# Kernel tuning notes

Hardware: AMD Instinct MI355X
Metric: run time of the kernel (lower is better)

Reference implementation:

```python
import jax, jax.numpy as jnp
import numpy as np

HID = 128
N_NODES = 50000
N_EDGES = 640000
N_GRAPHS = 64
N_LAYERS = 3
LN_EPS = 1e-5


def _ln(h, g, b):
    mu = jnp.mean(h, axis=-1, keepdims=True)
    v = jnp.mean(jnp.square(h - mu), axis=-1, keepdims=True)
    return (h - mu) * jax.lax.rsqrt(v + LN_EPS) * g + b


def _mlp2(h, W1, b1, g, be, W2, b2):
    # Linear -> ReLU -> LayerNorm -> (Dropout=identity in eval) -> Linear
    h = _ln(jax.nn.relu(h @ W1.T + b1), g, be)
    return h @ W2.T + b2


def _forward(x, edge_index, batch, axis_W1, axis_b1, axis_g, axis_be, axis_W2, axis_b2, org_W1, org_b1, org_g, org_be, org_W2, org_b2, nin_W, nin_b, conv_W1, conv_b1, conv_g, conv_be, conv_W2, conv_b2, eps, ln_g, ln_b, gate_W1, gate_b1, gate_g, gate_be, gate_W2, gate_b2, head_W1, head_b1, head_g, head_be, head_W2, head_b2):
    axis = x[:, 9:12]
    origin = x[:, 12:15]
    others = jnp.concatenate([x[:, :9], x[:, 15:19]], axis=1)  # [N, 13]
    axis_z = _mlp2(axis, axis_W1, axis_b1, axis_g, axis_be, axis_W2, axis_b2)
    org_z = _mlp2(origin, org_W1, org_b1, org_g, org_be, org_W2, org_b2)
    h = jnp.concatenate([others, axis_z, org_z], axis=1) @ nin_W.T + nin_b  # [N, HID]
    src, dst = edge_index[0], edge_index[1]
    n = x.shape[0]
    for l in range(N_LAYERS):
        res = h
        # GIN: sum-aggregate source features into targets (gather + scatter-add)
        agg = jax.ops.segment_sum(h[src], dst, num_segments=n)
        m = (1.0 + eps[l]) * h + agg
        m = _mlp2(m, conv_W1[l], conv_b1[l], conv_g[l], conv_be[l], conv_W2[l], conv_b2[l])
        h = _ln(jax.nn.relu(m), ln_g[l], ln_b[l]) + res
    # AttentionalAggregation: segment softmax over per-graph node gates
    gate = _mlp2(h, gate_W1, gate_b1, gate_g, gate_be, gate_W2, gate_b2)  # [N, 1]
    gmax = jax.ops.segment_max(gate, batch, num_segments=N_GRAPHS)
    e = jnp.exp(gate - gmax[batch])
    denom = jax.ops.segment_sum(e, batch, num_segments=N_GRAPHS)
    attn = e / denom[batch]
    g = jax.ops.segment_sum(attn * h, batch, num_segments=N_GRAPHS)  # [B, HID]
    logit = _mlp2(g, head_W1, head_b1, head_g, head_be, head_W2, head_b2)[:, 0]
    return logit


def setup_inputs() -> dict:
    key = jax.random.key(0)
    ks = iter(jax.random.split(key, 64))
    nk = lambda: next(ks)
    lin = lambda o, i: jax.random.normal(nk(), (o, i), jnp.float32) / np.float32(np.sqrt(i))
    lin3 = lambda L, o, i: jnp.stack([lin(o, i) for _ in range(L)])
    z = lambda *s: jnp.zeros(s, jnp.float32)
    o = lambda *s: jnp.ones(s, jnp.float32)
    inp = {}
    inp['x'] = jax.random.normal(nk(), (N_NODES, 19), jnp.float32)
    inp['edge_index'] = jax.random.randint(nk(), (2, N_EDGES), 0, N_NODES)
    inp['batch'] = jnp.sort(jax.random.randint(nk(), (N_NODES,), 0, N_GRAPHS))
    for p in ('axis', 'org'):
        inp[p + '_W1'] = lin(16, 3); inp[p + '_b1'] = z(16)
        inp[p + '_g'] = o(16); inp[p + '_be'] = z(16)
        inp[p + '_W2'] = lin(16, 16); inp[p + '_b2'] = z(16)
    inp['nin_W'] = lin(HID, 45); inp['nin_b'] = z(HID)
    inp['conv_W1'] = lin3(N_LAYERS, HID, HID); inp['conv_b1'] = z(N_LAYERS, HID)
    inp['conv_g'] = o(N_LAYERS, HID); inp['conv_be'] = z(N_LAYERS, HID)
    inp['conv_W2'] = lin3(N_LAYERS, HID, HID); inp['conv_b2'] = z(N_LAYERS, HID)
    inp['eps'] = z(N_LAYERS)
    inp['ln_g'] = o(N_LAYERS, HID); inp['ln_b'] = z(N_LAYERS, HID)
    for p in ('gate', 'head'):
        inp[p + '_W1'] = lin(HID // 2, HID); inp[p + '_b1'] = z(HID // 2)
        inp[p + '_g'] = o(HID // 2); inp[p + '_be'] = z(HID // 2)
        inp[p + '_W2'] = lin(1, HID // 2); inp[p + '_b2'] = z(1)
    return inp


def reference(x, edge_index, batch, axis_W1, axis_b1, axis_g, axis_be, axis_W2, axis_b2, org_W1, org_b1, org_g, org_be, org_W2, org_b2, nin_W, nin_b, conv_W1, conv_b1, conv_g, conv_be, conv_W2, conv_b2, eps, ln_g, ln_b, gate_W1, gate_b1, gate_g, gate_be, gate_W2, gate_b2, head_W1, head_b1, head_g, head_be, head_W2, head_b2):
    return _forward(x, edge_index, batch, axis_W1, axis_b1, axis_g, axis_be, axis_W2, axis_b2, org_W1, org_b1, org_g, org_be, org_W2, org_b2, nin_W, nin_b, conv_W1, conv_b1, conv_g, conv_be, conv_W2, conv_b2, eps, ln_g, ln_b, gate_W1, gate_b1, gate_g, gate_be, gate_W2, gate_b2, head_W1, head_b1, head_g, head_be, head_W2, head_b2)
```

## Files before the change

kernel.cpp:

```cpp
#include <hip/hip_runtime.h>

#define N_NODESC 50000
#define N_EDGESC 640000
#define N_GRAPHSC 64
#define HIDC 128
#define LN_EPSF 1e-5f
#define POOL_SPLIT 16
#define SCAN_NB 49
#define EGRID ((N_EDGESC + 255) / 256)
#define NGRID_GB ((N_NODESC + 255) / 256)
#define WPREP_NB 32

typedef short bf16x8 __attribute__((ext_vector_type(8)));
typedef float f32x4 __attribute__((ext_vector_type(4)));

static __device__ __forceinline__ unsigned ord_enc(float f) {
  unsigned u = __float_as_uint(f);
  return (u & 0x80000000u) ? ~u : (u | 0x80000000u);
}
static __device__ __forceinline__ float ord_dec(unsigned u) {
  return __uint_as_float((u & 0x80000000u) ? (u ^ 0x80000000u) : ~u);
}
static __device__ __forceinline__ unsigned short f2bf(float x) {
  unsigned u = __float_as_uint(x);
  u += 0x7fffu + ((u >> 16) & 1u);
  return (unsigned short)(u >> 16);
}
static __device__ __forceinline__ float bf2f(unsigned short b) {
  return __uint_as_float(((unsigned)b) << 16);
}

static __device__ __forceinline__ void mlp16(float in0, float in1, float in2,
    const float* __restrict__ W1, const float* __restrict__ b1,
    const float* __restrict__ g, const float* __restrict__ be,
    const float* __restrict__ W2, const float* __restrict__ b2,
    float* __restrict__ out) {
  float h[16];
  float s1 = 0.f, s2 = 0.f;
#pragma unroll
  for (int j = 0; j < 16; ++j) {
    float v = b1[j] + W1[j*3+0]*in0 + W1[j*3+1]*in1 + W1[j*3+2]*in2;
    v = fmaxf(v, 0.f);
    h[j] = v; s1 += v; s2 += v*v;
  }
  float mu = s1 * (1.f/16.f);
  float var = fmaxf(s2 * (1.f/16.f) - mu*mu, 0.f);
  float rs = rsqrtf(var + LN_EPSF);
  float z[16];
#pragma unroll
  for (int j = 0; j < 16; ++j) z[j] = (h[j]-mu)*rs*g[j] + be[j];
#pragma unroll
  for (int j = 0; j < 16; ++j) {
    float v = b2[j];
#pragma unroll
    for (int k = 0; k < 16; ++k) v += W2[j*16+k]*z[k];
    out[j] = v;
  }
}

__global__ __launch_bounds__(256) void hist_gbound_kernel(const int* __restrict__ ei,
    int* __restrict__ deg, const int* __restrict__ batch, int* __restrict__ gstart,
    const float* __restrict__ ninW, unsigned short* __restrict__ ninWb) {
  const int b = blockIdx.x;
  if (b < EGRID) {
    int e = b * 256 + threadIdx.x;
    if (e < N_EDGESC) atomicAdd(&deg[ei[N_EDGESC + e]], 1);
  } else if (b < EGRID + NGRID_GB) {
    int i = (b - EGRID) * 256 + threadIdx.x;
    if (i >= N_NODESC) return;
    int bb = batch[i];
    int prev = (i == 0) ? -1 : batch[i-1];
    for (int g = prev + 1; g <= bb; ++g) gstart[g] = i;
    if (i == N_NODESC - 1) {
      for (int g = bb + 1; g <= N_GRAPHSC; ++g) gstart[g] = N_NODESC;
    }
  } else {
    int i = (b - EGRID - NGRID_GB) * 256 + threadIdx.x;
    if (i < 128*64) {
      int f = i >> 6, k = i & 63;
      ninWb[i] = (k < 45) ? f2bf(ninW[f*45 + k]) : (unsigned short)0;
    }
  }
}

__global__ __launch_bounds__(1024) void scan1_kernel(const int* __restrict__ deg,
                                                     int* __restrict__ incl,
                                                     int* __restrict__ bsum) {
  const int b = blockIdx.x, t = threadIdx.x;
  const int i = b * 1024 + t;
  const int lane = t & 63, w = t >> 6;
  int v = (i < N_NODESC) ? deg[i] : 0;
#pragma unroll
  for (int off = 1; off < 64; off <<= 1) {
    int n = __shfl_up(v, off);
    if (lane >= off) v += n;
  }
  __shared__ int wsum[16];
  if (lane == 63) wsum[w] = v;
  __syncthreads();
  if (t == 0) {
    int run = 0;
#pragma unroll
    for (int k = 0; k < 16; ++k) { int x = wsum[k]; wsum[k] = run; run += x; }
  }
  __syncthreads();
  v += wsum[w];
  if (i < N_NODESC) incl[i] = v;
  if (t == 1023) bsum[b] = v;
}

__global__ __launch_bounds__(1024) void scan23_kernel(const int* __restrict__ deg,
                                                      const int* __restrict__ bsum,
                                                      int* __restrict__ rowptr,
                                                      int* __restrict__ cursor) {
  __shared__ int ex[SCAN_NB + 1];
  const int b = blockIdx.x, t = threadIdx.x;
  if (t < 64) {
    int v = (t < SCAN_NB) ? bsum[t] : 0;
    const int orig = v;
#pragma unroll
    for (int off = 1; off < 64; off <<= 1) {
      int n = __shfl_up(v, off);
      if (t >= off) v += n;
    }
    if (t < SCAN_NB) ex[t] = v - orig;
    if (t == SCAN_NB - 1) ex[SCAN_NB] = v;
  }
  __syncthreads();
  const int i = b * 1024 + t;
  if (i < N_NODESC) {
    int excl = rowptr[i] - deg[i] + ex[b];
    rowptr[i] = excl;
    cursor[i] = excl;
  }
  if (b == 0 && t == 0) rowptr[N_NODESC] = ex[SCAN_NB];
}

__global__ __launch_bounds__(256) void scatter_kernel(const int* __restrict__ ei,
                                                      int* __restrict__ cursor,
                                                      int* __restrict__ esrc) {
  int e = blockIdx.x * 256 + threadIdx.x;
  if (e < N_EDGESC) {
    int d = ei[N_EDGESC + e];
    int slot = atomicAdd(&cursor[d], 1);
    esrc[slot] = ei[e];
  }
}

__global__ __launch_bounds__(256, 4) void enc_mfma_kernel(
    const float* __restrict__ x,
    const float* __restrict__ aW1, const float* __restrict__ ab1,
    const float* __restrict__ ag,  const float* __restrict__ abe,
    const float* __restrict__ aW2, const float* __restrict__ ab2,
    const float* __restrict__ oW1, const float* __restrict__ ob1,
    const float* __restrict__ og,  const float* __restrict__ obe,
    const float* __restrict__ oW2, const float* __restrict__ ob2,
    const unsigned short* __restrict__ ninWb, const float* __restrict__ ninb,
    unsigned short* __restrict__ Hb) {
  __shared__ unsigned short Ab[64*136];
  const int t = threadIdx.x;
  const int nb = blockIdx.x * 64;

  if (t < 64) {
    const int gn = nb + t;
    unsigned short row[64];
    if (gn < N_NODESC) {
      float in45[45];
      const float* xr = x + gn * 19;
#pragma unroll
      for (int k = 0; k < 9; ++k) in45[k] = xr[k];
#pragma unroll
      for (int k = 0; k < 4; ++k) in45[9+k] = xr[15+k];
      mlp16(xr[9], xr[10], xr[11], aW1, ab1, ag, abe, aW2, ab2, &in45[13]);
      mlp16(xr[12], xr[13], xr[14], oW1, ob1, og, obe, oW2, ob2, &in45[29]);
#pragma unroll
      for (int k = 0; k < 45; ++k) row[k] = f2bf(in45[k]);
#pragma unroll
      for (int k = 45; k < 64; ++k) row[k] = 0;
    } else {
#pragma unroll
      for (int k = 0; k < 64; ++k) row[k] = 0;
    }
#pragma unroll
    for (int k = 0; k < 64; ++k) Ab[t*136 + k] = row[k];
  }
  __syncthreads();

  const int lane = t & 63, wv = t >> 6;
  const int quad = lane >> 4, l16 = lane & 15;
  const int arow = (wv*16 + l16)*136 + quad*8;
  f32x4 acc[8];
#pragma unroll
  for (int ft = 0; ft < 8; ++ft) acc[ft] = (f32x4){0.f,0.f,0.f,0.f};
#pragma unroll
  for (int ks = 0; ks < 2; ++ks) {
    bf16x8 a = *(const bf16x8*)(const void*)&Ab[arow + ks*32];
#pragma unroll
    for (int ft = 0; ft < 8; ++ft) {
      bf16x8 bfr = *(const bf16x8*)&ninWb[(ft*16 + l16)*64 + quad*8 + ks*32];
      acc[ft] = __builtin_amdgcn_mfma_f32_16x16x32_bf16(a, bfr, acc[ft], 0, 0, 0);
    }
  }
  float bb[8];
#pragma unroll
  for (int ft = 0; ft < 8; ++ft) bb[ft] = ninb[ft*16 + l16];
  __syncthreads();
#pragma unroll
  for (int r = 0; r < 4; ++r) {
    int nloc = wv*16 + quad*4 + r;
#pragma unroll
    for (int ft = 0; ft < 8; ++ft)
      Ab[nloc*136 + ft*16 + l16] = f2bf(acc[ft][r] + bb[ft]);
  }
  __syncthreads();
#pragma unroll
  for (int i = 0; i < 4; ++i) {
    int chunk = t + i*256;
    int n = chunk >> 4, c8 = chunk & 15;
    int gn = nb + n;
    if (gn < N_NODESC)
      *(bf16x8*)&Hb[gn*HIDC + c8*8] = *(const bf16x8*)&Ab[n*136 + c8*8];
  }
}

__global__ __launch_bounds__(256, 3) void conv_fused_kernel(
    const unsigned short* __restrict__ Hin,
    const int* __restrict__ rowptr, const int* __restrict__ esrc,
    const float* __restrict__ epsp,
    const float* __restrict__ W1, const float* __restrict__ b1,
    const float* __restrict__ g1, const float* __restrict__ be1,
    const float* __restrict__ W2, const float* __restrict__ b2,
    const float* __restrict__ lng, const float* __restrict__ lnb,
    unsigned short* __restrict__ Hout) {
  __shared__ unsigned short Ab[64*136];
  __shared__ unsigned short Wl[128*136];
  const int t = threadIdx.x;
  const int nb = blockIdx.x * 64;

#pragma unroll
  for (int i = 0; i < 16; ++i) {
    int q = t + i*256;
    int f = q >> 5, c4 = q & 31;
    float4 v = *(const float4*)&W1[f*HIDC + c4*4];
    ushort4 h;
    h.x = f2bf(v.x); h.y = f2bf(v.y); h.z = f2bf(v.z); h.w = f2bf(v.w);
    *(ushort4*)&Wl[f*136 + c4*4] = h;
  }

  {
    const float e1 = 1.0f + epsp[0];
    const int v64 = t >> 2;
    const int c   = t & 3;
    const int node = nb + v64;
    if (node < N_NODESC) {
      const unsigned short* __restrict__ hrow = &Hin[node*HIDC + c*32];
      float acc[4][8];
#pragma unroll
      for (int j = 0; j < 4; ++j)
#pragma unroll
        for (int k = 0; k < 8; ++k) acc[j][k] = 0.f;
      int s = rowptr[node];
      const int e = rowptr[node+1];
      for (; s + 2 <= e; s += 2) {
        int i0 = esrc[s], i1 = esrc[s+1];
        const unsigned short* r0 = &Hin[i0*HIDC + c*32];
        const unsigned short* r1 = &Hin[i1*HIDC + c*32];
        bf16x8 x00 = *(const bf16x8*)&r0[0],  x01 = *(const bf16x8*)&r0[8];
        bf16x8 x02 = *(const bf16x8*)&r0[16], x03 = *(const bf16x8*)&r0[24];
        bf16x8 x10 = *(const bf16x8*)&r1[0],  x11 = *(const bf16x8*)&r1[8];
        bf16x8 x12 = *(const bf16x8*)&r1[16], x13 = *(const bf16x8*)&r1[24];
#pragma unroll
        for (int k = 0; k < 8; ++k) {
          acc[0][k] += bf2f((unsigned short)x00[k]) + bf2f((unsigned short)x10[k]);
          acc[1][k] += bf2f((unsigned short)x01[k]) + bf2f((unsigned short)x11[k]);
          acc[2][k] += bf2f((unsigned short)x02[k]) + bf2f((unsigned short)x12[k]);
          acc[3][k] += bf2f((unsigned short)x03[k]) + bf2f((unsigned short)x13[k]);
        }
      }
      if (s < e) {
        const unsigned short* r0 = &Hin[esrc[s]*HIDC + c*32];
        bf16x8 x00 = *(const bf16x8*)&r0[0],  x01 = *(const bf16x8*)&r0[8];
        bf16x8 x02 = *(const bf16x8*)&r0[16], x03 = *(const bf16x8*)&r0[24];
#pragma unroll
        for (int k = 0; k < 8; ++k) {
          acc[0][k] += bf2f((unsigned short)x00[k]);
          acc[1][k] += bf2f((unsigned short)x01[k]);
          acc[2][k] += bf2f((unsigned short)x02[k]);
          acc[3][k] += bf2f((unsigned short)x03[k]);
        }
      }
#pragma unroll
      for (int j = 0; j < 4; ++j) {
        bf16x8 h = *(const bf16x8*)&hrow[j*8];
        bf16x8 m8;
#pragma unroll
        for (int k = 0; k < 8; ++k)
          m8[k] = (short)f2bf(e1*bf2f((unsigned short)h[k]) + acc[j][k]);
        *(bf16x8*)&Ab[v64*136 + c*32 + j*8] = m8;
      }
    } else {
#pragma unroll
      for (int j = 0; j < 4; ++j)
        *(bf16x8*)&Ab[v64*136 + c*32 + j*8] = (bf16x8){0,0,0,0,0,0,0,0};
    }
  }
  __syncthreads();

  const int lane = t & 63, wv = t >> 6;
  const int quad = lane >> 4, l16 = lane & 15;
  const int arow = (wv*16 + l16)*136 + quad*8;

  f32x4 acc[8];
#pragma unroll
  for (int ft = 0; ft < 8; ++ft) acc[ft] = (f32x4){0.f,0.f,0.f,0.f};
#pragma unroll
  for (int ks = 0; ks < 4; ++ks) {
    bf16x8 a = *(const bf16x8*)(const void*)&Ab[arow + ks*32];
#pragma unroll
    for (int ft = 0; ft < 8; ++ft) {
      bf16x8 b = *(const bf16x8*)(const void*)&Wl[(ft*16 + l16)*136 + quad*8 + ks*32];
      acc[ft] = __builtin_amdgcn_mfma_f32_16x16x32_bf16(a, b, acc[ft], 0, 0, 0);
    }
  }

  {
    float bb[8], gg[8], bee[8];
#pragma unroll
    for (int ft = 0; ft < 8; ++ft) {
      int f = ft*16 + l16;
      bb[ft] = b1[f]; gg[ft] = g1[f]; bee[ft] = be1[f];
    }
    float s1[4] = {0,0,0,0}, s2[4] = {0,0,0,0};
#pragma unroll
    for (int ft = 0; ft < 8; ++ft)
#pragma unroll
      for (int r = 0; r < 4; ++r) {
        float v = fmaxf(acc[ft][r] + bb[ft], 0.f);
        acc[ft][r] = v; s1[r] += v; s2[r] += v*v;
      }
#pragma unroll
    for (int m = 1; m < 16; m <<= 1)
#pragma unroll
      for (int r = 0; r < 4; ++r) {
        s1[r] += __shfl_xor(s1[r], m);
        s2[r] += __shfl_xor(s2[r], m);
      }
    float mu[4], rs[4];
#pragma unroll
    for (int r = 0; r < 4; ++r) {
      mu[r] = s1[r] * (1.f/128.f);
      float var = fmaxf(s2[r] * (1.f/128.f) - mu[r]*mu[r], 0.f);
      rs[r] = rsqrtf(var + LN_EPSF);
    }
    __syncthreads();
#pragma unroll
    for (int r = 0; r < 4; ++r) {
      int nloc = wv*16 + quad*4 + r;
#pragma unroll
      for (int ft = 0; ft < 8; ++ft) {
        float o = (acc[ft][r] - mu[r])*rs[r]*gg[ft] + bee[ft];
        Ab[nloc*136 + ft*16 + l16] = f2bf(o);
      }
    }
  }
#pragma unroll
  for (int i = 0; i < 16; ++i) {
    int q = t + i*256;
    int f = q >> 5, c4 = q & 31;
    float4 v = *(const float4*)&W2[f*HIDC + c4*4];
    ushort4 h;
    h.x = f2bf(v.x); h.y = f2bf(v.y); h.z = f2bf(v.z); h.w = f2bf(v.w);
    *(ushort4*)&Wl[f*136 + c4*4] = h;
  }
  __syncthreads();

#pragma unroll
  for (int ft = 0; ft < 8; ++ft) acc[ft] = (f32x4){0.f,0.f,0.f,0.f};
#pragma unroll
  for (int ks = 0; ks < 4; ++ks) {
    bf16x8 a = *(const bf16x8*)(const void*)&Ab[arow + ks*32];
#pragma unroll
    for (int ft = 0; ft < 8; ++ft) {
      bf16x8 b = *(const bf16x8*)(const void*)&Wl[(ft*16 + l16)*136 + quad*8 + ks*32];
      acc[ft] = __builtin_amdgcn_mfma_f32_16x16x32_bf16(a, b, acc[ft], 0, 0, 0);
    }
  }

  {
    float bb[8], gg[8], bee[8];
#pragma unroll
    for (int ft = 0; ft < 8; ++ft) {
      int f = ft*16 + l16;
      bb[ft] = b2[f]; gg[ft] = lng[f]; bee[ft] = lnb[f];
    }
    float s1[4] = {0,0,0,0}, s2[4] = {0,0,0,0};
#pragma unroll
    for (int ft = 0; ft < 8; ++ft)
#pragma unroll
      for (int r = 0; r < 4; ++r) {
        float v = fmaxf(acc[ft][r] + bb[ft], 0.f);
        acc[ft][r] = v; s1[r] += v; s2[r] += v*v;
      }
#pragma unroll
    for (int m = 1; m < 16; m <<= 1)
#pragma unroll
      for (int r = 0; r < 4; ++r) {
        s1[r] += __shfl_xor(s1[r], m);
        s2[r] += __shfl_xor(s2[r], m);
      }
    float mu[4], rs[4];
#pragma unroll
    for (int r = 0; r < 4; ++r) {
      mu[r] = s1[r] * (1.f/128.f);
      float var = fmaxf(s2[r] * (1.f/128.f) - mu[r]*mu[r], 0.f);
      rs[r] = rsqrtf(var + LN_EPSF);
    }
    __syncthreads();
#pragma unroll
    for (int r = 0; r < 4; ++r) {
      int nloc = wv*16 + quad*4 + r;
#pragma unroll
      for (int ft = 0; ft < 8; ++ft) {
        float o = (acc[ft][r] - mu[r])*rs[r]*gg[ft] + bee[ft];
        Ab[nloc*136 + ft*16 + l16] = f2bf(o);
      }
    }
  }
  __syncthreads();
#pragma unroll
  for (int i = 0; i < 4; ++i) {
    int chunk = t + i*256;
    int n = chunk >> 4, cc = chunk & 15;
    int gn = nb + n;
    if (gn >= N_NODESC) continue;
    bf16x8 vv = *(const bf16x8*)&Ab[n*136 + cc*8];
    bf16x8 rr = *(const bf16x8*)&Hin[gn*HIDC + cc*8];
    bf16x8 o8;
#pragma unroll
    for (int k = 0; k < 8; ++k)
      o8[k] = (short)f2bf(bf2f((unsigned short)vv[k]) + bf2f((unsigned short)rr[k]));
    *(bf16x8*)&Hout[gn*HIDC + cc*8] = o8;
  }
}

__global__ __launch_bounds__(256, 4) void gate_mfma_kernel(
    const unsigned short* __restrict__ Hb, const float* __restrict__ W1,
    const float* __restrict__ b1, const float* __restrict__ lng,
    const float* __restrict__ lnb, const float* __restrict__ W2,
    const float* __restrict__ b2, const int* __restrict__ batch,
    float* __restrict__ gateb, unsigned* __restrict__ gmaxu) {
  __shared__ unsigned short Ab[64*136];
  __shared__ unsigned short Wl[64*136];
  __shared__ unsigned sgm[N_GRAPHSC];
  const int t = threadIdx.x;
  const int nb = blockIdx.x * 64;
  if (t < N_GRAPHSC) sgm[t] = 0u;
#pragma unroll
  for (int i = 0; i < 4; ++i) {
    int chunk = t + i*256;
    int n = chunk >> 4, c8 = chunk & 15;
    int gn = nb + n;
    bf16x8 v = {0,0,0,0,0,0,0,0};
    if (gn < N_NODESC) v = *(const bf16x8*)&Hb[gn*HIDC + c8*8];
    *(bf16x8*)&Ab[n*136 + c8*8] = v;
  }
#pragma unroll
  for (int i = 0; i < 8; ++i) {
    int q = t + i*256;
    int f = q >> 5, c4 = q & 31;
    float4 v = *(const float4*)&W1[f*HIDC + c4*4];
    ushort4 h;
    h.x = f2bf(v.x); h.y = f2bf(v.y); h.z = f2bf(v.z); h.w = f2bf(v.w);
    *(ushort4*)&Wl[f*136 + c4*4] = h;
  }
  __syncthreads();

  const int lane = t & 63, wv = t >> 6;
  const int quad = lane >> 4, l16 = lane & 15;
  f32x4 acc[4];
#pragma unroll
  for (int ft = 0; ft < 4; ++ft) acc[ft] = (f32x4){0.f,0.f,0.f,0.f};

  const int arow = (wv*16 + l16)*136 + quad*8;
#pragma unroll
  for (int ks = 0; ks < 4; ++ks) {
    bf16x8 a = *(const bf16x8*)(const void*)&Ab[arow + ks*32];
#pragma unroll
    for (int ft = 0; ft < 4; ++ft) {
      bf16x8 b = *(const bf16x8*)(const void*)&Wl[(ft*16 + l16)*136 + quad*8 + ks*32];
      acc[ft] = __builtin_amdgcn_mfma_f32_16x16x32_bf16(a, b, acc[ft], 0, 0, 0);
    }
  }

  float bb[4], gg[4], bee[4], w2v[4];
#pragma unroll
  for (int ft = 0; ft < 4; ++ft) {
    int f = ft*16 + l16;
    bb[ft] = b1[f]; gg[ft] = lng[f]; bee[ft] = lnb[f]; w2v[ft] = W2[f];
  }
  float s1[4] = {0,0,0,0}, s2[4] = {0,0,0,0};
#pragma unroll
  for (int ft = 0; ft < 4; ++ft)
#pragma unroll
    for (int r = 0; r < 4; ++r) {
      float v = fmaxf(acc[ft][r] + bb[ft], 0.f);
      acc[ft][r] = v; s1[r] += v; s2[r] += v*v;
    }
#pragma unroll
  for (int m = 1; m < 16; m <<= 1)
#pragma unroll
    for (int r = 0; r < 4; ++r) {
      s1[r] += __shfl_xor(s1[r], m);
      s2[r] += __shfl_xor(s2[r], m);
    }
  float pd[4];
#pragma unroll
  for (int r = 0; r < 4; ++r) {
    float mu = s1[r] * (1.f/64.f);
    float var = fmaxf(s2[r] * (1.f/64.f) - mu*mu, 0.f);
    float rs = rsqrtf(var + LN_EPSF);
    float p = 0.f;
#pragma unroll
    for (int ft = 0; ft < 4; ++ft)
      p += ((acc[ft][r] - mu)*rs*gg[ft] + bee[ft]) * w2v[ft];
    pd[r] = p;
  }
#pragma unroll
  for (int m = 1; m < 16; m <<= 1)
#pragma unroll
    for (int r = 0; r < 4; ++r) pd[r] += __shfl_xor(pd[r], m);
  if (l16 == 0) {
    float b2v = b2[0];
#pragma unroll
    for (int r = 0; r < 4; ++r) {
      int node = nb + wv*16 + quad*4 + r;
      if (node < N_NODESC) {
        float gv = pd[r] + b2v;
        gateb[node] = gv;
        atomicMax(&sgm[batch[node]], ord_enc(gv));
      }
    }
  }
  __syncthreads();
  if (t < N_GRAPHSC && sgm[t] != 0u) atomicMax(&gmaxu[t], sgm[t]);
}

__global__ __launch_bounds__(256) void pool_kernel(const unsigned short* __restrict__ Hb,
    const float* __restrict__ gateb, const int* __restrict__ gstart,
    const unsigned* __restrict__ gmaxu, float* __restrict__ S,
    float* __restrict__ denom) {
  const int g    = blockIdx.x / POOL_SPLIT;
  const int part = blockIdx.x % POOL_SPLIT;
  const int s0 = gstart[g], s1 = gstart[g+1];
  const int cnt = s1 - s0;
  const int chunk = (cnt + POOL_SPLIT - 1) / POOL_SPLIT;
  int lo = s0 + part * chunk;
  int hi = lo + chunk; if (hi > s1) hi = s1;
  const int t = threadIdx.x;
  const int c8 = t & 15;
  const int v  = t >> 4;
  const float gm = ord_dec(gmaxu[g]);
  float acc[8];
#pragma unroll
  for (int k = 0; k < 8; ++k) acc[k] = 0.f;
  float de = 0.f;
  for (int n = lo + v; n < hi; n += 16) {
    float e = expf(gateb[n] - gm);
    bf16x8 hv = *(const bf16x8*)&Hb[n*HIDC + c8*8];
#pragma unroll
    for (int k = 0; k < 8; ++k) acc[k] += e * bf2f((unsigned short)hv[k]);
    if (c8 == 0) de += e;
  }
  __shared__ float sacc[16*128];
  __shared__ float sden[16];
#pragma unroll
  for (int k = 0; k < 8; ++k) sacc[v*128 + c8*8 + k] = acc[k];
  if (c8 == 0) sden[v] = de;
  __syncthreads();
  if (t < 128) {
    float s = 0.f;
#pragma unroll
    for (int vv = 0; vv < 16; ++vv) s += sacc[vv*128 + t];
    atomicAdd(&S[g*HIDC + t], s);
  }
  if (t == 0) {
    float d = 0.f;
#pragma unroll
    for (int vv = 0; vv < 16; ++vv) d += sden[vv];
    atomicAdd(&denom[g], d);
  }
}

__global__ __launch_bounds__(64) void head_kernel(const float* __restrict__ S,
    const float* __restrict__ denom, const float* __restrict__ W1,
    const float* __restrict__ b1, const float* __restrict__ g,
    const float* __restrict__ be, const float* __restrict__ W2,
    const float* __restrict__ b2, float* __restrict__ out) {
  const int gr = blockIdx.x;
  const int j = threadIdx.x;
  const float inv = 1.0f / denom[gr];
  float v = b1[j];
  for (int k = 0; k < HIDC; ++k) v += (S[gr*HIDC + k] * inv) * W1[j*HIDC + k];
  v = fmaxf(v, 0.f);
  float s1 = v, s2 = v*v;
  for (int off = 32; off; off >>= 1) { s1 += __shfl_xor(s1, off); s2 += __shfl_xor(s2, off); }
  float mu = s1 * (1.f/64.f);
  float var = fmaxf(s2 * (1.f/64.f) - mu*mu, 0.f);
  float rs = rsqrtf(var + LN_EPSF);
  float z = (v-mu)*rs*g[j] + be[j];
  float p = z * W2[j];
  for (int off = 32; off; off >>= 1) p += __shfl_xor(p, off);
  if (j == 0) out[gr] = p + b2[0];
}

extern "C" void kernel_launch(void* const* d_in, const int* in_sizes, int n_in,
                              void* d_out, int out_size, void* d_ws, size_t ws_size,
                              hipStream_t stream) {
  (void)in_sizes; (void)n_in; (void)out_size; (void)ws_size;
  const float* x     = (const float*)d_in[0];
  const int*   ei    = (const int*)d_in[1];
  const int*   batch = (const int*)d_in[2];
  const float* aW1 = (const float*)d_in[3];
  const float* ab1 = (const float*)d_in[4];
  const float* ag  = (const float*)d_in[5];
  const float* abe = (const float*)d_in[6];
  const float* aW2 = (const float*)d_in[7];
  const float* ab2 = (const float*)d_in[8];
  const float* oW1 = (const float*)d_in[9];
  const float* ob1 = (const float*)d_in[10];
  const float* og  = (const float*)d_in[11];
  const float* obe = (const float*)d_in[12];
  const float* oW2 = (const float*)d_in[13];
  const float* ob2 = (const float*)d_in[14];
  const float* ninW = (const float*)d_in[15];
  const float* ninb = (const float*)d_in[16];
  const float* cW1 = (const float*)d_in[17];
  const float* cb1 = (const float*)d_in[18];
  const float* cg  = (const float*)d_in[19];
  const float* cbe = (const float*)d_in[20];
  const float* cW2 = (const float*)d_in[21];
  const float* cb2 = (const float*)d_in[22];
  const float* eps = (const float*)d_in[23];
  const float* lng = (const float*)d_in[24];
  const float* lnb = (const float*)d_in[25];
  const float* gW1 = (const float*)d_in[26];
  const float* gb1 = (const float*)d_in[27];
  const float* gg  = (const float*)d_in[28];
  const float* gbe = (const float*)d_in[29];
  const float* gW2 = (const float*)d_in[30];
  const float* gb2 = (const float*)d_in[31];
  const float* hW1 = (const float*)d_in[32];
  const float* hb1 = (const float*)d_in[33];
  const float* hg  = (const float*)d_in[34];
  const float* hbe = (const float*)d_in[35];
  const float* hW2 = (const float*)d_in[36];
  const float* hb2 = (const float*)d_in[37];

  char* ws = (char*)d_ws;
  unsigned short* Ha = (unsigned short*)(ws + 0);
  unsigned short* Hc = (unsigned short*)(ws + 12800000);
  float* gateb = (float*)(ws + 25600000);
  int*   deg   = (int*)(ws + 25800000);
  float* S     = (float*)(ws + 26000000);
  float* denom = (float*)(ws + 26032768);
  unsigned* gmaxu = (unsigned*)(ws + 26033024);
  int* rowptr  = (int*)(ws + 26033280);
  int* cursor  = (int*)(ws + 26233284);
  int* esrc    = (int*)(ws + 26433284);
  int* bsum    = (int*)(ws + 28993284);
  int* gstart  = (int*)(ws + 28993540);
  unsigned short* ninWb = (unsigned short*)(ws + 29000000);

  hipMemsetAsync(deg, 0, 233280, stream);

  hist_gbound_kernel<<<EGRID + NGRID_GB + WPREP_NB, 256, 0, stream>>>(
      ei, deg, batch, gstart, ninW, ninWb);
  scan1_kernel<<<SCAN_NB, 1024, 0, stream>>>(deg, rowptr, bsum);
  scan23_kernel<<<SCAN_NB, 1024, 0, stream>>>(deg, bsum, rowptr, cursor);
  scatter_kernel<<<EGRID, 256, 0, stream>>>(ei, cursor, esrc);

  const int ngrid64 = (N_NODESC + 63) / 64;
  enc_mfma_kernel<<<ngrid64, 256, 0, stream>>>(x, aW1, ab1, ag, abe, aW2, ab2,
                                               oW1, ob1, og, obe, oW2, ob2,
                                               ninWb, ninb, Ha);
  unsigned short* cur = Ha;
  unsigned short* nxt = Hc;
  for (int l = 0; l < 3; ++l) {
    conv_fused_kernel<<<ngrid64, 256, 0, stream>>>(
        cur, rowptr, esrc, eps + l,
        cW1 + l*HIDC*HIDC, cb1 + l*HIDC, cg + l*HIDC, cbe + l*HIDC,
        cW2 + l*HIDC*HIDC, cb2 + l*HIDC, lng + l*HIDC, lnb + l*HIDC,
        nxt);
    unsigned short* tmp = cur; cur = nxt; nxt = tmp;
  }
  gate_mfma_kernel<<<ngrid64, 256, 0, stream>>>(cur, gW1, gb1, gg, gbe, gW2, gb2,
                                                batch, gateb, gmaxu);
  pool_kernel<<<N_GRAPHSC * POOL_SPLIT, 256, 0, stream>>>(cur, gateb, gstart, gmaxu, S, denom);
  head_kernel<<<N_GRAPHSC, 64, 0, stream>>>(S, denom, hW1, hb1, hg, hbe, hW2, hb2,
                                            (float*)d_out);
}
```

Before: 387.9 us.

## Split GIN conv into separate aggregation and GEMM kernels, prequantize conv weights

The fused conv kernel is split in two. A lightweight aggregation kernel uses 16 lanes per node and 4-way unrolled gathers to build the (1+eps)h+agg message into a bf16 buffer. A GEMM-pair kernel then runs the two MLP matmuls. Conv weights are converted to bf16 once in the prep kernel instead of per block, and the encoder spreads its two small MLPs across three thread groups. This trades an extra round trip of the message tensor through memory and extra launches for better latency hiding in the gather and less per-block weight conversion.

```diff
diff --git a/kernel.cpp b/kernel.cpp
--- a/kernel.cpp
+++ b/kernel.cpp
@@ -9,7 +9,8 @@
 #define SCAN_NB 49
 #define EGRID ((N_EDGESC + 255) / 256)
 #define NGRID_GB ((N_NODESC + 255) / 256)
-#define WPREP_NB 32
+#define PREP_ELEMS (8192 + 49152 + 49152)
+#define WPREP_NB ((PREP_ELEMS + 255) / 256)
 
 typedef short bf16x8 __attribute__((ext_vector_type(8)));
 typedef float f32x4 __attribute__((ext_vector_type(4)));
@@ -60,7 +61,9 @@
 
 __global__ __launch_bounds__(256) void hist_gbound_kernel(const int* __restrict__ ei,
     int* __restrict__ deg, const int* __restrict__ batch, int* __restrict__ gstart,
-    const float* __restrict__ ninW, unsigned short* __restrict__ ninWb) {
+    const float* __restrict__ ninW, unsigned short* __restrict__ ninWb,
+    const float* __restrict__ cW1, unsigned short* __restrict__ cW1b,
+    const float* __restrict__ cW2, unsigned short* __restrict__ cW2b) {
   const int b = blockIdx.x;
   if (b < EGRID) {
     int e = b * 256 + threadIdx.x;
@@ -76,9 +79,15 @@
     }
   } else {
     int i = (b - EGRID - NGRID_GB) * 256 + threadIdx.x;
-    if (i < 128*64) {
+    if (i < 8192) {
       int f = i >> 6, k = i & 63;
       ninWb[i] = (k < 45) ? f2bf(ninW[f*45 + k]) : (unsigned short)0;
+    } else if (i < 8192 + 49152) {
+      int j = i - 8192;
+      cW1b[j] = f2bf(cW1[j]);
+    } else if (i < PREP_ELEMS) {
+      int j = i - 8192 - 49152;
+      cW2b[j] = f2bf(cW2[j]);
     }
   }
 }
@@ -161,28 +170,44 @@
   const int t = threadIdx.x;
   const int nb = blockIdx.x * 64;
 
-  if (t < 64) {
-    const int gn = nb + t;
-    unsigned short row[64];
+  if (t < 192) {
+    const int n = t & 63;
+    const int gn = nb + n;
+    const int grp = t >> 6;
     if (gn < N_NODESC) {
-      float in45[45];
       const float* xr = x + gn * 19;
-#pragma unroll
-      for (int k = 0; k < 9; ++k) in45[k] = xr[k];
-#pragma unroll
-      for (int k = 0; k < 4; ++k) in45[9+k] = xr[15+k];
-      mlp16(xr[9], xr[10], xr[11], aW1, ab1, ag, abe, aW2, ab2, &in45[13]);
-      mlp16(xr[12], xr[13], xr[14], oW1, ob1, og, obe, oW2, ob2, &in45[29]);
-#pragma unroll
-      for (int k = 0; k < 45; ++k) row[k] = f2bf(in45[k]);
-#pragma unroll
-      for (int k = 45; k < 64; ++k) row[k] = 0;
+      if (grp == 0) {
+        float z[16];
+        mlp16(xr[9], xr[10], xr[11], aW1, ab1, ag, abe, aW2, ab2, z);
+#pragma unroll
+        for (int k = 0; k < 16; ++k) Ab[n*136 + 13 + k] = f2bf(z[k]);
+      } else if (grp == 1) {
+        float z[16];
+        mlp16(xr[12], xr[13], xr[14], oW1, ob1, og, obe, oW2, ob2, z);
+#pragma unroll
+        for (int k = 0; k < 16; ++k) Ab[n*136 + 29 + k] = f2bf(z[k]);
+      } else {
+#pragma unroll
+        for (int k = 0; k < 9; ++k) Ab[n*136 + k] = f2bf(xr[k]);
+#pragma unroll
+        for (int k = 0; k < 4; ++k) Ab[n*136 + 9 + k] = f2bf(xr[15 + k]);
+#pragma unroll
+        for (int k = 45; k < 64; ++k) Ab[n*136 + k] = 0;
+      }
     } else {
-#pragma unroll
-      for (int k = 0; k < 64; ++k) row[k] = 0;
-    }
-#pragma unroll
-    for (int k = 0; k < 64; ++k) Ab[t*136 + k] = row[k];
+      if (grp == 0) {
+#pragma unroll
+        for (int k = 0; k < 16; ++k) Ab[n*136 + 13 + k] = 0;
+      } else if (grp == 1) {
+#pragma unroll
+        for (int k = 0; k < 16; ++k) Ab[n*136 + 29 + k] = 0;
+      } else {
+#pragma unroll
+        for (int k = 0; k < 13; ++k) Ab[n*136 + k] = 0;
+#pragma unroll
+        for (int k = 45; k < 64; ++k) Ab[n*136 + k] = 0;
+      }
+    }
   }
   __syncthreads();
 
@@ -223,13 +248,50 @@
   }
 }
 
-__global__ __launch_bounds__(256, 3) void conv_fused_kernel(
+__global__ __launch_bounds__(128) void agg_kernel(const unsigned short* __restrict__ Hb,
+    const int* __restrict__ rowptr, const int* __restrict__ esrc,
+    const float* __restrict__ epsp, unsigned short* __restrict__ Mb) {
+  const int t = threadIdx.x;
+  const int c8 = t & 15;
+  const int v  = t >> 4;
+  const int node = blockIdx.x * 8 + v;
+  if (node >= N_NODESC) return;
+  const float e1 = 1.0f + epsp[0];
+  bf16x8 h = *(const bf16x8*)&Hb[node*HIDC + c8*8];
+  float acc[8];
+#pragma unroll
+  for (int k = 0; k < 8; ++k) acc[k] = 0.f;
+  int s = rowptr[node];
+  const int e = rowptr[node+1];
+  for (; s + 4 <= e; s += 4) {
+    int i0 = esrc[s], i1 = esrc[s+1], i2 = esrc[s+2], i3 = esrc[s+3];
+    bf16x8 x0 = *(const bf16x8*)&Hb[i0*HIDC + c8*8];
+    bf16x8 x1 = *(const bf16x8*)&Hb[i1*HIDC + c8*8];
+    bf16x8 x2 = *(const bf16x8*)&Hb[i2*HIDC + c8*8];
+    bf16x8 x3 = *(const bf16x8*)&Hb[i3*HIDC + c8*8];
+#pragma unroll
+    for (int k = 0; k < 8; ++k)
+      acc[k] += (bf2f((unsigned short)x0[k]) + bf2f((unsigned short)x1[k]))
+              + (bf2f((unsigned short)x2[k]) + bf2f((unsigned short)x3[k]));
+  }
+  for (; s < e; ++s) {
+    bf16x8 x0 = *(const bf16x8*)&Hb[esrc[s]*HIDC + c8*8];
+#pragma unroll
+    for (int k = 0; k < 8; ++k) acc[k] += bf2f((unsigned short)x0[k]);
+  }
+  bf16x8 m8;
+#pragma unroll
+  for (int k = 0; k < 8; ++k)
+    m8[k] = (short)f2bf(e1*bf2f((unsigned short)h[k]) + acc[k]);
+  *(bf16x8*)&Mb[node*HIDC + c8*8] = m8;
+}
+
+__global__ __launch_bounds__(256, 3) void gemmpair_kernel(
+    const unsigned short* __restrict__ Mb,
     const unsigned short* __restrict__ Hin,
-    const int* __restrict__ rowptr, const int* __restrict__ esrc,
-    const float* __restrict__ epsp,
-    const float* __restrict__ W1, const float* __restrict__ b1,
+    const unsigned short* __restrict__ W1b, const float* __restrict__ b1,
     const float* __restrict__ g1, const float* __restrict__ be1,
-    const float* __restrict__ W2, const float* __restrict__ b2,
+    const unsigned short* __restrict__ W2b, const float* __restrict__ b2,
     const float* __restrict__ lng, const float* __restrict__ lnb,
     unsigned short* __restrict__ Hout) {
   __shared__ unsigned short Ab[64*136];
@@ -238,71 +300,19 @@
   const int nb = blockIdx.x * 64;
 
 #pragma unroll
-  for (int i = 0; i < 16; ++i) {
+  for (int i = 0; i < 4; ++i) {
+    int chunk = t + i*256;
+    int n = chunk >> 4, c8 = chunk & 15;
+    int gn = nb + n;
+    bf16x8 v = {0,0,0,0,0,0,0,0};
+    if (gn < N_NODESC) v = *(const bf16x8*)&Mb[gn*HIDC + c8*8];
+    *(bf16x8*)&Ab[n*136 + c8*8] = v;
+  }
+#pragma unroll
+  for (int i = 0; i < 8; ++i) {
     int q = t + i*256;
-    int f = q >> 5, c4 = q & 31;
-    float4 v = *(const float4*)&W1[f*HIDC + c4*4];
-    ushort4 h;
-    h.x = f2bf(v.x); h.y = f2bf(v.y); h.z = f2bf(v.z); h.w = f2bf(v.w);
-    *(ushort4*)&Wl[f*136 + c4*4] = h;
-  }
-
-  {
-    const float e1 = 1.0f + epsp[0];
-    const int v64 = t >> 2;
-    const int c   = t & 3;
-    const int node = nb + v64;
-    if (node < N_NODESC) {
-      const unsigned short* __restrict__ hrow = &Hin[node*HIDC + c*32];
-      float acc[4][8];
-#pragma unroll
-      for (int j = 0; j < 4; ++j)
-#pragma unroll
-        for (int k = 0; k < 8; ++k) acc[j][k] = 0.f;
-      int s = rowptr[node];
-      const int e = rowptr[node+1];
-      for (; s + 2 <= e; s += 2) {
-        int i0 = esrc[s], i1 = esrc[s+1];
-        const unsigned short* r0 = &Hin[i0*HIDC + c*32];
-        const unsigned short* r1 = &Hin[i1*HIDC + c*32];
-        bf16x8 x00 = *(const bf16x8*)&r0[0],  x01 = *(const bf16x8*)&r0[8];
-        bf16x8 x02 = *(const bf16x8*)&r0[16], x03 = *(const bf16x8*)&r0[24];
-        bf16x8 x10 = *(const bf16x8*)&r1[0],  x11 = *(const bf16x8*)&r1[8];
-        bf16x8 x12 = *(const bf16x8*)&r1[16], x13 = *(const bf16x8*)&r1[24];
-#pragma unroll
-        for (int k = 0; k < 8; ++k) {
-          acc[0][k] += bf2f((unsigned short)x00[k]) + bf2f((unsigned short)x10[k]);
-          acc[1][k] += bf2f((unsigned short)x01[k]) + bf2f((unsigned short)x11[k]);
-          acc[2][k] += bf2f((unsigned short)x02[k]) + bf2f((unsigned short)x12[k]);
-          acc[3][k] += bf2f((unsigned short)x03[k]) + bf2f((unsigned short)x13[k]);
-        }
-      }
-      if (s < e) {
-        const unsigned short* r0 = &Hin[esrc[s]*HIDC + c*32];
-        bf16x8 x00 = *(const bf16x8*)&r0[0],  x01 = *(const bf16x8*)&r0[8];
-        bf16x8 x02 = *(const bf16x8*)&r0[16], x03 = *(const bf16x8*)&r0[24];
-#pragma unroll
-        for (int k = 0; k < 8; ++k) {
-          acc[0][k] += bf2f((unsigned short)x00[k]);
-          acc[1][k] += bf2f((unsigned short)x01[k]);
-          acc[2][k] += bf2f((unsigned short)x02[k]);
-          acc[3][k] += bf2f((unsigned short)x03[k]);
-        }
-      }
-#pragma unroll
-      for (int j = 0; j < 4; ++j) {
-        bf16x8 h = *(const bf16x8*)&hrow[j*8];
-        bf16x8 m8;
-#pragma unroll
-        for (int k = 0; k < 8; ++k)
-          m8[k] = (short)f2bf(e1*bf2f((unsigned short)h[k]) + acc[j][k]);
-        *(bf16x8*)&Ab[v64*136 + c*32 + j*8] = m8;
-      }
-    } else {
-#pragma unroll
-      for (int j = 0; j < 4; ++j)
-        *(bf16x8*)&Ab[v64*136 + c*32 + j*8] = (bf16x8){0,0,0,0,0,0,0,0};
-    }
+    int f = q >> 4, c8 = q & 15;
+    *(bf16x8*)&Wl[f*136 + c8*8] = *(const bf16x8*)&W1b[f*HIDC + c8*8];
   }
   __syncthreads();
 
@@ -364,13 +374,10 @@
     }
   }
 #pragma unroll
-  for (int i = 0; i < 16; ++i) {
+  for (int i = 0; i < 8; ++i) {
     int q = t + i*256;
-    int f = q >> 5, c4 = q & 31;
-    float4 v = *(const float4*)&W2[f*HIDC + c4*4];
-    ushort4 h;
-    h.x = f2bf(v.x); h.y = f2bf(v.y); h.z = f2bf(v.z); h.w = f2bf(v.w);
-    *(ushort4*)&Wl[f*136 + c4*4] = h;
+    int f = q >> 4, c8 = q & 15;
+    *(bf16x8*)&Wl[f*136 + c8*8] = *(const bf16x8*)&W2b[f*HIDC + c8*8];
   }
   __syncthreads();
 
@@ -659,22 +666,25 @@
   char* ws = (char*)d_ws;
   unsigned short* Ha = (unsigned short*)(ws + 0);
   unsigned short* Hc = (unsigned short*)(ws + 12800000);
-  float* gateb = (float*)(ws + 25600000);
-  int*   deg   = (int*)(ws + 25800000);
-  float* S     = (float*)(ws + 26000000);
-  float* denom = (float*)(ws + 26032768);
-  unsigned* gmaxu = (unsigned*)(ws + 26033024);
-  int* rowptr  = (int*)(ws + 26033280);
-  int* cursor  = (int*)(ws + 26233284);
-  int* esrc    = (int*)(ws + 26433284);
-  int* bsum    = (int*)(ws + 28993284);
-  int* gstart  = (int*)(ws + 28993540);
-  unsigned short* ninWb = (unsigned short*)(ws + 29000000);
+  unsigned short* Mb = (unsigned short*)(ws + 25600000);
+  float* gateb = (float*)(ws + 38400000);
+  int*   deg   = (int*)(ws + 38600000);
+  float* S     = (float*)(ws + 38800000);
+  float* denom = (float*)(ws + 38832768);
+  unsigned* gmaxu = (unsigned*)(ws + 38833024);
+  int* rowptr  = (int*)(ws + 38833280);
+  int* cursor  = (int*)(ws + 39033284);
+  int* esrc    = (int*)(ws + 39233284);
+  int* bsum    = (int*)(ws + 41793284);
+  int* gstart  = (int*)(ws + 41793540);
+  unsigned short* ninWb = (unsigned short*)(ws + 41800000);
+  unsigned short* cW1b  = (unsigned short*)(ws + 41816384);
+  unsigned short* cW2b  = (unsigned short*)(ws + 41914688);
 
   hipMemsetAsync(deg, 0, 233280, stream);
 
   hist_gbound_kernel<<<EGRID + NGRID_GB + WPREP_NB, 256, 0, stream>>>(
-      ei, deg, batch, gstart, ninW, ninWb);
+      ei, deg, batch, gstart, ninW, ninWb, cW1, cW1b, cW2, cW2b);
   scan1_kernel<<<SCAN_NB, 1024, 0, stream>>>(deg, rowptr, bsum);
   scan23_kernel<<<SCAN_NB, 1024, 0, stream>>>(deg, bsum, rowptr, cursor);
   scatter_kernel<<<EGRID, 256, 0, stream>>>(ei, cursor, esrc);
@@ -686,10 +696,11 @@
   unsigned short* cur = Ha;
   unsigned short* nxt = Hc;
   for (int l = 0; l < 3; ++l) {
-    conv_fused_kernel<<<ngrid64, 256, 0, stream>>>(
-        cur, rowptr, esrc, eps + l,
-        cW1 + l*HIDC*HIDC, cb1 + l*HIDC, cg + l*HIDC, cbe + l*HIDC,
-        cW2 + l*HIDC*HIDC, cb2 + l*HIDC, lng + l*HIDC, lnb + l*HIDC,
+    agg_kernel<<<(N_NODESC + 7) / 8, 128, 0, stream>>>(cur, rowptr, esrc, eps + l, Mb);
+    gemmpair_kernel<<<ngrid64, 256, 0, stream>>>(
+        Mb, cur,
+        cW1b + l*HIDC*HIDC, cb1 + l*HIDC, cg + l*HIDC, cbe + l*HIDC,
+        cW2b + l*HIDC*HIDC, cb2 + l*HIDC, lng + l*HIDC, lnb + l*HIDC,
         nxt);
     unsigned short* tmp = cur; cur = nxt; nxt = tmp;
   }
```

New measurement: 373.7 us, median of 2. 1.04x faster.
